# Kernel optimization log

Hardware: AMD Instinct MI355X
Metric: run time of the kernel (lower is better)

## Reference

```python
import jax, jax.numpy as jnp
import numpy as np

STATE_DIM = 512
N_AGENTS = 16
N_ACTIONS = 32
EMBED = 512          # mixing_embed_dim
Q_IN = STATE_DIM + N_AGENTS * N_ACTIONS  # 1024 (coma_critic arch)
ROWS = 32768         # bs * ts = 64 * 512


def _linear_params(key, d_in, d_out):
    kw, kb = jax.random.split(key)
    bound = 1.0 / np.sqrt(d_in)
    W = jax.random.uniform(kw, (d_in, d_out), minval=-bound, maxval=bound, dtype=jnp.float32)
    b = jax.random.uniform(kb, (d_out,), minval=-bound, maxval=bound, dtype=jnp.float32)
    return W, b


def setup_inputs() -> dict:
    key = jax.random.key(0)
    ks = jax.random.split(key, 8)
    states = jax.random.normal(ks[0], (ROWS, STATE_DIM), dtype=jnp.float32)
    actions = jax.random.uniform(ks[1], (ROWS, N_AGENTS * N_ACTIONS), dtype=jnp.float32)
    Qw1, Qb1 = _linear_params(ks[2], Q_IN, EMBED)
    Qw2, Qb2 = _linear_params(ks[3], EMBED, EMBED)
    Qw3, Qb3 = _linear_params(ks[4], EMBED, 1)
    Vw1, Vb1 = _linear_params(ks[5], STATE_DIM, EMBED)
    Vw2, Vb2 = _linear_params(ks[6], EMBED, EMBED)
    Vw3, Vb3 = _linear_params(ks[7], EMBED, 1)
    return {
        "states": states, "actions": actions,
        "Qw1": Qw1, "Qb1": Qb1, "Qw2": Qw2, "Qb2": Qb2, "Qw3": Qw3, "Qb3": Qb3,
        "Vw1": Vw1, "Vb1": Vb1, "Vw2": Vw2, "Vb2": Vb2, "Vw3": Vw3, "Vb3": Vb3,
    }


def _mlp3(x, W1, b1, W2, b2, W3, b3):
    h = jax.nn.relu(x @ W1 + b1)
    h = jax.nn.relu(h @ W2 + b2)
    return h @ W3 + b3


def reference(states, actions,
              Qw1, Qb1, Qw2, Qb2, Qw3, Qb3,
              Vw1, Vb1, Vw2, Vb2, Vw3, Vb3):
    # coma_critic arch: inputs = cat([states, joint-action one-hots], dim=1)
    inputs = jnp.concatenate([states, actions], axis=1)  # [bs*ts, Q_IN]
    q_outputs = _mlp3(inputs, Qw1, Qb1, Qw2, Qb2, Qw3, Qb3)  # [bs*ts, 1]
    v_outputs = _mlp3(states, Vw1, Vb1, Vw2, Vb2, Vw3, Vb3)  # [bs*ts, 1]
    return q_outputs, v_outputs
```

## Files before the change

kernel.cpp:

```cpp
#include <hip/hip_runtime.h>


#define ROWS 32768
#define EMBED 512

using frag_ab = __attribute__((ext_vector_type(8))) short;
using f32x4   = __attribute__((ext_vector_type(4))) float;

__device__ __forceinline__ unsigned short f2bf(float f) {
    unsigned int u = __builtin_bit_cast(unsigned int, f);
    return (unsigned short)((u + 0x7fffu + ((u >> 16) & 1u)) >> 16);
}

__device__ __forceinline__ unsigned pk2rne(float lo, float hi) {
    return (unsigned)f2bf(lo) | ((unsigned)f2bf(hi) << 16);
}

__device__ __forceinline__ void async_copy16(const void* g, void* l) {
    __builtin_amdgcn_global_load_lds(
        (const __attribute__((address_space(1))) unsigned int*)g,
        (__attribute__((address_space(3))) unsigned int*)l, 16, 0, 0);
}

__device__ __forceinline__ void decode_mn(int L, int& mi, int& nq) {
    nq = (L >> 3) & 3;
    mi = ((L >> 5) << 3) | (L & 7);
}

__global__ __launch_bounds__(256)
void prep(const float* __restrict__ states, const float* __restrict__ actions,
          const float* __restrict__ Qw1, const float* __restrict__ Qw2,
          const float* __restrict__ Vw1, const float* __restrict__ Vw2,
          const float* __restrict__ qb3, const float* __restrict__ vb3,
          unsigned short* __restrict__ X,
          unsigned short* __restrict__ Qw1t, unsigned short* __restrict__ Qw2t,
          unsigned short* __restrict__ Vw1t, unsigned short* __restrict__ Vw2t,
          float* __restrict__ out) {
    const int b = blockIdx.x, tid = threadIdx.x;
    if (b < 4096) {
        int c = b * 256 + tid;
        int m = c >> 5, col = (c & 31) * 32;
        const float* src = (col < 512) ? states + (size_t)m * 512 + col
                                       : actions + (size_t)m * 512 + (col - 512);
        float4 f[8];
#pragma unroll
        for (int i = 0; i < 8; i++) f[i] = ((const float4*)src)[i];
        uint4* dst = (uint4*)(X + (size_t)m * 1024 + col);
#pragma unroll
        for (int i = 0; i < 4; i++)
            dst[i] = make_uint4(pk2rne(f[2*i].x,   f[2*i].y),
                                pk2rne(f[2*i].z,   f[2*i].w),
                                pk2rne(f[2*i+1].x, f[2*i+1].y),
                                pk2rne(f[2*i+1].z, f[2*i+1].w));
    } else if (b < 4736) {
        int g = (b - 4096) * 256 + tid;
        const float* W; unsigned short* O; int n, k0, ldo;
        if (g < 65536) {
            int o = g * 8; n = o >> 10; k0 = o & 1023; W = Qw1; O = Qw1t; ldo = 1024;
        } else {
            g -= 65536;
            int seg = g >> 15, r = g & 32767, o = r * 8;
            n = o >> 9; k0 = o & 511; ldo = 512;
            W = (seg == 0) ? Qw2 : (seg == 1) ? Vw1 : Vw2;
            O = (seg == 0) ? Qw2t : (seg == 1) ? Vw1t : Vw2t;
        }
        float v[8];
#pragma unroll
        for (int j = 0; j < 8; j++) v[j] = W[(size_t)(k0 + j) * 512 + n];
        *(uint4*)(O + (size_t)n * ldo + k0) =
            make_uint4(pk2rne(v[0], v[1]), pk2rne(v[2], v[3]),
                       pk2rne(v[4], v[5]), pk2rne(v[6], v[7]));
    } else {
        int i = (b - 4736) * 256 + tid;
        out[i] = (i < ROWS) ? qb3[0] : vb3[0];
    }
}

__global__ __launch_bounds__(256, 2)
void layer1(const unsigned short* __restrict__ X,
            const unsigned short* __restrict__ Qw1t,
            const unsigned short* __restrict__ Vw1t,
            const float* __restrict__ Qb1, const float* __restrict__ Vb1,
            unsigned short* __restrict__ h1Q, unsigned short* __restrict__ h1V) {
    __shared__ __align__(16) unsigned short As[2 * 4096];
    __shared__ __align__(16) unsigned short Bs[2 * 8192];

    const int tid = threadIdx.x, wave = tid >> 6, lane = tid & 63;
    int mi, nq; decode_mn(blockIdx.x, mi, nq);
    const bool isV = nq >= 2;
    const int bn = (nq & 1) * 256;
    const int bm = mi * 128;
    const int K = isV ? 512 : 1024;
    const unsigned short* Wt = isV ? Vw1t : Qw1t;
    const float* bias = isV ? Vb1 : Qb1;
    unsigned short* H = isV ? h1V : h1Q;

    const int wm = (wave & 1) * 64, wn = (wave >> 1) * 128;
    const int lrow = lane & 15, quad = lane >> 4;
    f32x4 acc[4][8] = {};

    const int lin  = wave * 1024 + lane * 16;
    const int rowS = lin >> 6, colS = (lin & 63) >> 1;
    const unsigned short* gA0 = X + (size_t)(bm + rowS)      * 1024 + colS;
    const unsigned short* gA1 = X + (size_t)(bm + rowS + 64) * 1024 + colS;
    const unsigned short* gB0 = Wt + (size_t)(bn + rowS)       * K + colS;
    const unsigned short* gB1 = Wt + (size_t)(bn + rowS + 64)  * K + colS;
    const unsigned short* gB2 = Wt + (size_t)(bn + rowS + 128) * K + colS;
    const unsigned short* gB3 = Wt + (size_t)(bn + rowS + 192) * K + colS;
    unsigned short* ldsA0 = As + wave * 512;
    unsigned short* ldsA1 = As + 2048 + wave * 512;
    unsigned short* ldsB0 = Bs + wave * 512;
    unsigned short* ldsB1 = Bs + 2048 + wave * 512;
    unsigned short* ldsB2 = Bs + 4096 + wave * 512;
    unsigned short* ldsB3 = Bs + 6144 + wave * 512;

    for (int k0 = 0; k0 < K; k0 += 64) {
        async_copy16(gA0,      ldsA0);
        async_copy16(gA0 + 32, ldsA0 + 4096);
        async_copy16(gA1,      ldsA1);
        async_copy16(gA1 + 32, ldsA1 + 4096);
        async_copy16(gB0,      ldsB0);
        async_copy16(gB0 + 32, ldsB0 + 8192);
        async_copy16(gB1,      ldsB1);
        async_copy16(gB1 + 32, ldsB1 + 8192);
        async_copy16(gB2,      ldsB2);
        async_copy16(gB2 + 32, ldsB2 + 8192);
        async_copy16(gB3,      ldsB3);
        async_copy16(gB3 + 32, ldsB3 + 8192);
        gA0 += 64; gA1 += 64; gB0 += 64; gB1 += 64; gB2 += 64; gB3 += 64;
        __syncthreads();

#pragma unroll
        for (int s = 0; s < 2; s++) {
            frag_ab af[4], bfr[8];
#pragma unroll
            for (int i = 0; i < 4; i++)
                af[i] = *(const frag_ab*)&As[s * 4096 + (wm + i * 16 + lrow) * 32 + quad * 8];
#pragma unroll
            for (int j = 0; j < 8; j++)
                bfr[j] = *(const frag_ab*)&Bs[s * 8192 + (wn + j * 16 + lrow) * 32 + quad * 8];
#pragma unroll
            for (int i = 0; i < 4; i++)
#pragma unroll
                for (int j = 0; j < 8; j++)
                    acc[i][j] = __builtin_amdgcn_mfma_f32_16x16x32_bf16(
                        af[i], bfr[j], acc[i][j], 0, 0, 0);
        }
        __syncthreads();
    }

#pragma unroll
    for (int j = 0; j < 8; j++) {
        const int col = bn + wn + j * 16 + lrow;
        const float bc = bias[col];
#pragma unroll
        for (int i = 0; i < 4; i++) {
            const int row0 = bm + wm + i * 16 + quad * 4;
#pragma unroll
            for (int r = 0; r < 4; r++) {
                float v = acc[i][j][r] + bc;
                v = v > 0.0f ? v : 0.0f;
                H[(size_t)(row0 + r) * EMBED + col] = f2bf(v);
            }
        }
    }
}

__global__ __launch_bounds__(256, 2)
void layer2(const unsigned short* __restrict__ h1Q,
            const unsigned short* __restrict__ h1V,
            const unsigned short* __restrict__ Qw2t,
            const unsigned short* __restrict__ Vw2t,
            const float* __restrict__ Qb2, const float* __restrict__ Vb2,
            const float* __restrict__ Qw3, const float* __restrict__ Vw3,
            float* __restrict__ out) {
    __shared__ __align__(16) unsigned short As[2 * 4096];
    __shared__ __align__(16) unsigned short Bs[2 * 8192];

    const int tid = threadIdx.x, wave = tid >> 6, lane = tid & 63;
    int mi, nq; decode_mn(blockIdx.x, mi, nq);
    const bool isV = nq >= 2;
    const int bn = (nq & 1) * 256;
    const int bm = mi * 128;
    const unsigned short* A  = isV ? h1V : h1Q;
    const unsigned short* Wt = isV ? Vw2t : Qw2t;
    const float* bias = isV ? Vb2 : Qb2;
    const float* w3   = isV ? Vw3 : Qw3;
    float* op = out + (isV ? ROWS : 0);

    const int wm = (wave & 1) * 64, wn = (wave >> 1) * 128;
    const int lrow = lane & 15, quad = lane >> 4;
    f32x4 acc[4][8] = {};

    const int lin  = wave * 1024 + lane * 16;
    const int rowS = lin >> 6, colS = (lin & 63) >> 1;
    const unsigned short* gA0 = A + (size_t)(bm + rowS)      * 512 + colS;
    const unsigned short* gA1 = A + (size_t)(bm + rowS + 64) * 512 + colS;
    const unsigned short* gB0 = Wt + (size_t)(bn + rowS)       * 512 + colS;
    const unsigned short* gB1 = Wt + (size_t)(bn + rowS + 64)  * 512 + colS;
    const unsigned short* gB2 = Wt + (size_t)(bn + rowS + 128) * 512 + colS;
    const unsigned short* gB3 = Wt + (size_t)(bn + rowS + 192) * 512 + colS;
    unsigned short* ldsA0 = As + wave * 512;
    unsigned short* ldsA1 = As + 2048 + wave * 512;
    unsigned short* ldsB0 = Bs + wave * 512;
    unsigned short* ldsB1 = Bs + 2048 + wave * 512;
    unsigned short* ldsB2 = Bs + 4096 + wave * 512;
    unsigned short* ldsB3 = Bs + 6144 + wave * 512;

    for (int k0 = 0; k0 < 512; k0 += 64) {
        async_copy16(gA0,      ldsA0);
        async_copy16(gA0 + 32, ldsA0 + 4096);
        async_copy16(gA1,      ldsA1);
        async_copy16(gA1 + 32, ldsA1 + 4096);
        async_copy16(gB0,      ldsB0);
        async_copy16(gB0 + 32, ldsB0 + 8192);
        async_copy16(gB1,      ldsB1);
        async_copy16(gB1 + 32, ldsB1 + 8192);
        async_copy16(gB2,      ldsB2);
        async_copy16(gB2 + 32, ldsB2 + 8192);
        async_copy16(gB3,      ldsB3);
        async_copy16(gB3 + 32, ldsB3 + 8192);
        gA0 += 64; gA1 += 64; gB0 += 64; gB1 += 64; gB2 += 64; gB3 += 64;
        __syncthreads();

#pragma unroll
        for (int s = 0; s < 2; s++) {
            frag_ab af[4], bfr[8];
#pragma unroll
            for (int i = 0; i < 4; i++)
                af[i] = *(const frag_ab*)&As[s * 4096 + (wm + i * 16 + lrow) * 32 + quad * 8];
#pragma unroll
            for (int j = 0; j < 8; j++)
                bfr[j] = *(const frag_ab*)&Bs[s * 8192 + (wn + j * 16 + lrow) * 32 + quad * 8];
#pragma unroll
            for (int i = 0; i < 4; i++)
#pragma unroll
                for (int j = 0; j < 8; j++)
                    acc[i][j] = __builtin_amdgcn_mfma_f32_16x16x32_bf16(
                        af[i], bfr[j], acc[i][j], 0, 0, 0);
        }
        __syncthreads();
    }

    float bc[8], wc[8];
#pragma unroll
    for (int j = 0; j < 8; j++) {
        const int col = bn + wn + j * 16 + lrow;
        bc[j] = bias[col];
        wc[j] = w3[col];
    }
#pragma unroll
    for (int i = 0; i < 4; i++) {
#pragma unroll
        for (int r = 0; r < 4; r++) {
            float s = 0.0f;
#pragma unroll
            for (int j = 0; j < 8; j++) {
                float v = acc[i][j][r] + bc[j];
                v = v > 0.0f ? v : 0.0f;
                s += v * wc[j];
            }
#pragma unroll
            for (int m = 1; m < 16; m <<= 1) s += __shfl_xor(s, m, 64);
            if (lrow == 0)
                atomicAdd(&op[bm + wm + i * 16 + quad * 4 + r], s);
        }
    }
}

extern "C" void kernel_launch(void* const* d_in, const int* in_sizes, int n_in,
                              void* d_out, int out_size, void* d_ws, size_t ws_size,
                              hipStream_t stream) {
    const float* states  = (const float*)d_in[0];
    const float* actions = (const float*)d_in[1];
    const float* Qw1 = (const float*)d_in[2];
    const float* Qb1 = (const float*)d_in[3];
    const float* Qw2 = (const float*)d_in[4];
    const float* Qb2 = (const float*)d_in[5];
    const float* Qw3 = (const float*)d_in[6];
    const float* Qb3 = (const float*)d_in[7];
    const float* Vw1 = (const float*)d_in[8];
    const float* Vb1 = (const float*)d_in[9];
    const float* Vw2 = (const float*)d_in[10];
    const float* Vb2 = (const float*)d_in[11];
    const float* Vw3 = (const float*)d_in[12];
    const float* Vb3 = (const float*)d_in[13];
    float* out = (float*)d_out;

    char* ws = (char*)d_ws;
    unsigned short* X    = (unsigned short*)ws;
    unsigned short* h1Q  = (unsigned short*)(ws + 67108864);
    unsigned short* h1V  = (unsigned short*)(ws + 100663296);
    unsigned short* Qw1t = (unsigned short*)(ws + 134217728);
    unsigned short* Qw2t = Qw1t + 512 * 1024;
    unsigned short* Vw1t = Qw2t + 512 * 512;
    unsigned short* Vw2t = Vw1t + 512 * 512;

    prep<<<dim3(4992), dim3(256), 0, stream>>>(states, actions, Qw1, Qw2, Vw1, Vw2,
                                               Qb3, Vb3, X, Qw1t, Qw2t, Vw1t, Vw2t, out);

    layer1<<<dim3(1024), dim3(256), 0, stream>>>(X, Qw1t, Vw1t, Qb1, Vb1, h1Q, h1V);
    layer2<<<dim3(1024), dim3(256), 0, stream>>>(h1Q, h1V, Qw2t, Vw2t, Qb2, Vb2, Qw3, Vw3, out);
}
```

Measured before the change: 287.7 us.

## Rewrite GEMMs with 256x256 tiles, swizzled double-buffered LDS, and tiled weight transpose

The layer1 and layer2 GEMMs now use a shared 256x256-tile routine run by 512 threads. It double-buffers 128KB of LDS with XOR-swizzled rows to avoid bank conflicts, and interleaves the staging of the next tile with four quarter-MFMA phases that raise wave priority. Weight transposition in prep now goes through a 64x64 shared-memory tile, so global reads and writes are coalesced instead of strided. The block-to-work mapping also changes to group tiles. The risks are 128KB of LDS per block, which limits occupancy to one block per CU despite the launch bound, and heavy barrier use.

```diff
diff --git a/kernel.cpp b/kernel.cpp
--- a/kernel.cpp
+++ b/kernel.cpp
@@ -22,10 +22,10 @@
         (__attribute__((address_space(3))) unsigned int*)l, 16, 0, 0);
 }
 
-__device__ __forceinline__ void decode_mn(int L, int& mi, int& nq) {
-    nq = (L >> 3) & 3;
-    mi = ((L >> 5) << 3) | (L & 7);
-}
+#define VM0()   asm volatile("s_waitcnt vmcnt(0)" ::: "memory")
+#define LGKM0() asm volatile("s_waitcnt lgkmcnt(0)" ::: "memory")
+#define SBAR()  __builtin_amdgcn_s_barrier()
+#define SCHED0() __builtin_amdgcn_sched_barrier(0)
 
 __global__ __launch_bounds__(256)
 void prep(const float* __restrict__ states, const float* __restrict__ actions,
@@ -52,121 +52,189 @@
                                 pk2rne(f[2*i].z,   f[2*i].w),
                                 pk2rne(f[2*i+1].x, f[2*i+1].y),
                                 pk2rne(f[2*i+1].z, f[2*i+1].w));
-    } else if (b < 4736) {
-        int g = (b - 4096) * 256 + tid;
-        const float* W; unsigned short* O; int n, k0, ldo;
-        if (g < 65536) {
-            int o = g * 8; n = o >> 10; k0 = o & 1023; W = Qw1; O = Qw1t; ldo = 1024;
-        } else {
-            g -= 65536;
-            int seg = g >> 15, r = g & 32767, o = r * 8;
-            n = o >> 9; k0 = o & 511; ldo = 512;
+    } else if (b < 4416) {
+        __shared__ float T[64][65];
+        int tg = b - 4096;
+        const float* W; unsigned short* O; int Krows, kt, nt;
+        if (tg < 128) { W = Qw1; O = Qw1t; Krows = 1024; kt = tg >> 3; nt = tg & 7; }
+        else {
+            tg -= 128; int seg = tg >> 6, r = tg & 63;
+            kt = r >> 3; nt = r & 7; Krows = 512;
             W = (seg == 0) ? Qw2 : (seg == 1) ? Vw1 : Vw2;
             O = (seg == 0) ? Qw2t : (seg == 1) ? Vw1t : Vw2t;
         }
-        float v[8];
-#pragma unroll
-        for (int j = 0; j < 8; j++) v[j] = W[(size_t)(k0 + j) * 512 + n];
-        *(uint4*)(O + (size_t)n * ldo + k0) =
-            make_uint4(pk2rne(v[0], v[1]), pk2rne(v[2], v[3]),
-                       pk2rne(v[4], v[5]), pk2rne(v[6], v[7]));
+        const int k0 = kt * 64, n0 = nt * 64;
+        const int rr = tid >> 4, c4 = (tid & 15) * 4;
+#pragma unroll
+        for (int p = 0; p < 4; ++p) {
+            float4 v = *(const float4*)&W[(size_t)(k0 + p * 16 + rr) * 512 + n0 + c4];
+            T[p * 16 + rr][c4]     = v.x;
+            T[p * 16 + rr][c4 + 1] = v.y;
+            T[p * 16 + rr][c4 + 2] = v.z;
+            T[p * 16 + rr][c4 + 3] = v.w;
+        }
+        __syncthreads();
+        const int n = tid >> 2, kc = (tid & 3) * 16;
+        unsigned pk[8];
+#pragma unroll
+        for (int j = 0; j < 8; ++j)
+            pk[j] = pk2rne(T[kc + 2 * j][n], T[kc + 2 * j + 1][n]);
+        uint4* dst = (uint4*)(O + (size_t)(n0 + n) * Krows + k0 + kc);
+        dst[0] = make_uint4(pk[0], pk[1], pk[2], pk[3]);
+        dst[1] = make_uint4(pk[4], pk[5], pk[6], pk[7]);
     } else {
-        int i = (b - 4736) * 256 + tid;
+        int i = (b - 4416) * 256 + tid;
         out[i] = (i < ROWS) ? qb3[0] : vb3[0];
     }
 }
 
-__global__ __launch_bounds__(256, 2)
+__device__ __forceinline__ void gemm_256(
+    const unsigned short* __restrict__ A, int ldaE,
+    const unsigned short* __restrict__ Bt, int ldbE,
+    int K, int bm, int bn, char* smb, f32x4 acc[8][4])
+{
+    const int tid = threadIdx.x, wave = tid >> 6, lane = tid & 63;
+    const int im = wave >> 2, in = wave & 3;
+    const int lrow = lane & 15, quad = lane >> 4;
+    const int ldaB = ldaE * 2, ldbB = ldbE * 2;
+
+    const int srow = wave * 8 + (lane >> 3);
+    const int scol = (((lane & 7) ^ ((lane >> 3) & 7)) << 4);
+    const char* gA = (const char*)A + (size_t)(bm + srow) * ldaB + scol;
+    const char* gB = (const char*)Bt + (size_t)(bn + srow) * ldbB + scol;
+    char* ldsAw = smb + wave * 1024;
+    char* ldsBw = smb + 65536 + wave * 1024;
+
+    auto stageA = [&](int b, int h) {
+        const char* g = gA + (size_t)(h * 128) * ldaB;
+        char* l = ldsAw + b * 32768 + h * 16384;
+        async_copy16(g, l);
+        async_copy16(g + (size_t)64 * ldaB, l + 8192);
+    };
+    auto stageB = [&](int b, int h) {
+        const char* g = gB + (size_t)(h * 128) * ldbB;
+        char* l = ldsBw + b * 32768 + h * 16384;
+        async_copy16(g, l);
+        async_copy16(g + (size_t)64 * ldbB, l + 8192);
+    };
+
+    frag_ab a[4][2], b0[2][2], b1[2][2];
+
+    auto readA = [&](int b, int mh) {
+        const char* base = smb + b * 32768 + im * 16384;
+#pragma unroll
+        for (int i = 0; i < 4; ++i) {
+            const int r = mh * 64 + i * 16 + lrow;
+#pragma unroll
+            for (int s = 0; s < 2; ++s)
+                a[i][s] = *(const frag_ab*)(base + r * 128 +
+                              (((s * 4 + quad) ^ (r & 7)) << 4));
+        }
+    };
+    auto readB = [&](int b, int nh, frag_ab bb[2][2]) {
+#pragma unroll
+        for (int j = 0; j < 2; ++j) {
+            const int nr = in * 64 + nh * 32 + j * 16 + lrow;
+            const char* base = smb + 65536 + b * 32768 + (nr >> 7) * 16384;
+            const int r = nr & 127;
+#pragma unroll
+            for (int s = 0; s < 2; ++s)
+                bb[j][s] = *(const frag_ab*)(base + r * 128 +
+                               (((s * 4 + quad) ^ (r & 7)) << 4));
+        }
+    };
+    auto mma = [&](int mh, int nh, frag_ab bb[2][2]) {
+        __builtin_amdgcn_s_setprio(1);
+#pragma unroll
+        for (int s = 0; s < 2; ++s)
+#pragma unroll
+            for (int i = 0; i < 4; ++i)
+#pragma unroll
+                for (int j = 0; j < 2; ++j)
+                    acc[mh * 4 + i][nh * 2 + j] =
+                        __builtin_amdgcn_mfma_f32_16x16x32_bf16(
+                            a[i][s], bb[j][s], acc[mh * 4 + i][nh * 2 + j],
+                            0, 0, 0);
+        __builtin_amdgcn_s_setprio(0);
+    };
+
+    stageA(0, 0); stageB(0, 0); stageB(0, 1); stageA(0, 1);
+    gA += 128; gB += 128;
+    VM0();
+    SBAR();
+
+    const int NT = K >> 6;
+    int buf = 0;
+    for (int t = 0; t < NT; ++t) {
+        const bool more = (t + 1 < NT);
+        const int nb = buf ^ 1;
+        readA(buf, 0); readB(buf, 0, b0);
+        if (more) { stageA(nb, 0); stageB(nb, 0); }
+        SBAR(); LGKM0(); SCHED0();
+        mma(0, 0, b0);
+        SBAR();
+        readB(buf, 1, b1);
+        if (more) stageB(nb, 1);
+        SBAR(); LGKM0(); SCHED0();
+        mma(0, 1, b1);
+        SBAR();
+        readA(buf, 1);
+        if (more) { stageA(nb, 1); gA += 128; gB += 128; }
+        SBAR(); LGKM0(); SCHED0();
+        mma(1, 1, b1);
+        SBAR();
+        SBAR(); LGKM0(); SCHED0();
+        mma(1, 0, b0);
+        if (more) VM0();
+        SBAR();
+        buf ^= 1;
+    }
+}
+
+__device__ __forceinline__ void decode_work(int bid, int& mi, int& v) {
+    int work = ((bid & 7) << 6) | (bid >> 3);
+    mi = work >> 2; v = work & 3;
+}
+
+__global__ __launch_bounds__(512, 2)
 void layer1(const unsigned short* __restrict__ X,
             const unsigned short* __restrict__ Qw1t,
             const unsigned short* __restrict__ Vw1t,
             const float* __restrict__ Qb1, const float* __restrict__ Vb1,
             unsigned short* __restrict__ h1Q, unsigned short* __restrict__ h1V) {
-    __shared__ __align__(16) unsigned short As[2 * 4096];
-    __shared__ __align__(16) unsigned short Bs[2 * 8192];
-
-    const int tid = threadIdx.x, wave = tid >> 6, lane = tid & 63;
-    int mi, nq; decode_mn(blockIdx.x, mi, nq);
-    const bool isV = nq >= 2;
-    const int bn = (nq & 1) * 256;
-    const int bm = mi * 128;
+    __shared__ __align__(16) char smem[131072];
+    int mi, v; decode_work(blockIdx.x, mi, v);
+    const bool isV = v >= 2;
+    const int bm = mi * 256, bn = (v & 1) * 256;
     const int K = isV ? 512 : 1024;
     const unsigned short* Wt = isV ? Vw1t : Qw1t;
     const float* bias = isV ? Vb1 : Qb1;
     unsigned short* H = isV ? h1V : h1Q;
 
-    const int wm = (wave & 1) * 64, wn = (wave >> 1) * 128;
+    f32x4 acc[8][4] = {};
+    gemm_256(X, 1024, Wt, K, K, bm, bn, smem, acc);
+
+    const int tid = threadIdx.x, wave = tid >> 6, lane = tid & 63;
+    const int im = wave >> 2, in = wave & 3;
     const int lrow = lane & 15, quad = lane >> 4;
-    f32x4 acc[4][8] = {};
-
-    const int lin  = wave * 1024 + lane * 16;
-    const int rowS = lin >> 6, colS = (lin & 63) >> 1;
-    const unsigned short* gA0 = X + (size_t)(bm + rowS)      * 1024 + colS;
-    const unsigned short* gA1 = X + (size_t)(bm + rowS + 64) * 1024 + colS;
-    const unsigned short* gB0 = Wt + (size_t)(bn + rowS)       * K + colS;
-    const unsigned short* gB1 = Wt + (size_t)(bn + rowS + 64)  * K + colS;
-    const unsigned short* gB2 = Wt + (size_t)(bn + rowS + 128) * K + colS;
-    const unsigned short* gB3 = Wt + (size_t)(bn + rowS + 192) * K + colS;
-    unsigned short* ldsA0 = As + wave * 512;
-    unsigned short* ldsA1 = As + 2048 + wave * 512;
-    unsigned short* ldsB0 = Bs + wave * 512;
-    unsigned short* ldsB1 = Bs + 2048 + wave * 512;
-    unsigned short* ldsB2 = Bs + 4096 + wave * 512;
-    unsigned short* ldsB3 = Bs + 6144 + wave * 512;
-
-    for (int k0 = 0; k0 < K; k0 += 64) {
-        async_copy16(gA0,      ldsA0);
-        async_copy16(gA0 + 32, ldsA0 + 4096);
-        async_copy16(gA1,      ldsA1);
-        async_copy16(gA1 + 32, ldsA1 + 4096);
-        async_copy16(gB0,      ldsB0);
-        async_copy16(gB0 + 32, ldsB0 + 8192);
-        async_copy16(gB1,      ldsB1);
-        async_copy16(gB1 + 32, ldsB1 + 8192);
-        async_copy16(gB2,      ldsB2);
-        async_copy16(gB2 + 32, ldsB2 + 8192);
-        async_copy16(gB3,      ldsB3);
-        async_copy16(gB3 + 32, ldsB3 + 8192);
-        gA0 += 64; gA1 += 64; gB0 += 64; gB1 += 64; gB2 += 64; gB3 += 64;
-        __syncthreads();
-
-#pragma unroll
-        for (int s = 0; s < 2; s++) {
-            frag_ab af[4], bfr[8];
-#pragma unroll
-            for (int i = 0; i < 4; i++)
-                af[i] = *(const frag_ab*)&As[s * 4096 + (wm + i * 16 + lrow) * 32 + quad * 8];
-#pragma unroll
-            for (int j = 0; j < 8; j++)
-                bfr[j] = *(const frag_ab*)&Bs[s * 8192 + (wn + j * 16 + lrow) * 32 + quad * 8];
-#pragma unroll
-            for (int i = 0; i < 4; i++)
-#pragma unroll
-                for (int j = 0; j < 8; j++)
-                    acc[i][j] = __builtin_amdgcn_mfma_f32_16x16x32_bf16(
-                        af[i], bfr[j], acc[i][j], 0, 0, 0);
-        }
-        __syncthreads();
-    }
-
-#pragma unroll
-    for (int j = 0; j < 8; j++) {
-        const int col = bn + wn + j * 16 + lrow;
+#pragma unroll
+    for (int j = 0; j < 4; ++j) {
+        const int col = bn + in * 64 + j * 16 + lrow;
         const float bc = bias[col];
 #pragma unroll
-        for (int i = 0; i < 4; i++) {
-            const int row0 = bm + wm + i * 16 + quad * 4;
-#pragma unroll
-            for (int r = 0; r < 4; r++) {
-                float v = acc[i][j][r] + bc;
-                v = v > 0.0f ? v : 0.0f;
-                H[(size_t)(row0 + r) * EMBED + col] = f2bf(v);
+        for (int i = 0; i < 8; ++i) {
+            const int row0 = bm + im * 128 + i * 16 + quad * 4;
+#pragma unroll
+            for (int r = 0; r < 4; ++r) {
+                float val = acc[i][j][r] + bc;
+                val = val > 0.0f ? val : 0.0f;
+                H[(size_t)(row0 + r) * EMBED + col] = f2bf(val);
             }
         }
     }
 }
 
-__global__ __launch_bounds__(256, 2)
+__global__ __launch_bounds__(512, 2)
 void layer2(const unsigned short* __restrict__ h1Q,
             const unsigned short* __restrict__ h1V,
             const unsigned short* __restrict__ Qw2t,
@@ -174,96 +242,44 @@
             const float* __restrict__ Qb2, const float* __restrict__ Vb2,
             const float* __restrict__ Qw3, const float* __restrict__ Vw3,
             float* __restrict__ out) {
-    __shared__ __align__(16) unsigned short As[2 * 4096];
-    __shared__ __align__(16) unsigned short Bs[2 * 8192];
-
-    const int tid = threadIdx.x, wave = tid >> 6, lane = tid & 63;
-    int mi, nq; decode_mn(blockIdx.x, mi, nq);
-    const bool isV = nq >= 2;
-    const int bn = (nq & 1) * 256;
-    const int bm = mi * 128;
+    __shared__ __align__(16) char smem[131072];
+    int mi, v; decode_work(blockIdx.x, mi, v);
+    const bool isV = v >= 2;
+    const int bm = mi * 256, bn = (v & 1) * 256;
     const unsigned short* A  = isV ? h1V : h1Q;
     const unsigned short* Wt = isV ? Vw2t : Qw2t;
     const float* bias = isV ? Vb2 : Qb2;
     const float* w3   = isV ? Vw3 : Qw3;
     float* op = out + (isV ? ROWS : 0);
 
-    const int wm = (wave & 1) * 64, wn = (wave >> 1) * 128;
+    f32x4 acc[8][4] = {};
+    gemm_256(A, 512, Wt, 512, 512, bm, bn, smem, acc);
+
+    const int tid = threadIdx.x, wave = tid >> 6, lane = tid & 63;
+    const int im = wave >> 2, in = wave & 3;
     const int lrow = lane & 15, quad = lane >> 4;
-    f32x4 acc[4][8] = {};
-
-    const int lin  = wave * 1024 + lane * 16;
-    const int rowS = lin >> 6, colS = (lin & 63) >> 1;
-    const unsigned short* gA0 = A + (size_t)(bm + rowS)      * 512 + colS;
-    const unsigned short* gA1 = A + (size_t)(bm + rowS + 64) * 512 + colS;
-    const unsigned short* gB0 = Wt + (size_t)(bn + rowS)       * 512 + colS;
-    const unsigned short* gB1 = Wt + (size_t)(bn + rowS + 64)  * 512 + colS;
-    const unsigned short* gB2 = Wt + (size_t)(bn + rowS + 128) * 512 + colS;
-    const unsigned short* gB3 = Wt + (size_t)(bn + rowS + 192) * 512 + colS;
-    unsigned short* ldsA0 = As + wave * 512;
-    unsigned short* ldsA1 = As + 2048 + wave * 512;
-    unsigned short* ldsB0 = Bs + wave * 512;
-    unsigned short* ldsB1 = Bs + 2048 + wave * 512;
-    unsigned short* ldsB2 = Bs + 4096 + wave * 512;
-    unsigned short* ldsB3 = Bs + 6144 + wave * 512;
-
-    for (int k0 = 0; k0 < 512; k0 += 64) {
-        async_copy16(gA0,      ldsA0);
-        async_copy16(gA0 + 32, ldsA0 + 4096);
-        async_copy16(gA1,      ldsA1);
-        async_copy16(gA1 + 32, ldsA1 + 4096);
-        async_copy16(gB0,      ldsB0);
-        async_copy16(gB0 + 32, ldsB0 + 8192);
-        async_copy16(gB1,      ldsB1);
-        async_copy16(gB1 + 32, ldsB1 + 8192);
-        async_copy16(gB2,      ldsB2);
-        async_copy16(gB2 + 32, ldsB2 + 8192);
-        async_copy16(gB3,      ldsB3);
-        async_copy16(gB3 + 32, ldsB3 + 8192);
-        gA0 += 64; gA1 += 64; gB0 += 64; gB1 += 64; gB2 += 64; gB3 += 64;
-        __syncthreads();
-
-#pragma unroll
-        for (int s = 0; s < 2; s++) {
-            frag_ab af[4], bfr[8];
-#pragma unroll
-            for (int i = 0; i < 4; i++)
-                af[i] = *(const frag_ab*)&As[s * 4096 + (wm + i * 16 + lrow) * 32 + quad * 8];
-#pragma unroll
-            for (int j = 0; j < 8; j++)
-                bfr[j] = *(const frag_ab*)&Bs[s * 8192 + (wn + j * 16 + lrow) * 32 + quad * 8];
-#pragma unroll
-            for (int i = 0; i < 4; i++)
-#pragma unroll
-                for (int j = 0; j < 8; j++)
-                    acc[i][j] = __builtin_amdgcn_mfma_f32_16x16x32_bf16(
-                        af[i], bfr[j], acc[i][j], 0, 0, 0);
-        }
-        __syncthreads();
-    }
-
-    float bc[8], wc[8];
-#pragma unroll
-    for (int j = 0; j < 8; j++) {
-        const int col = bn + wn + j * 16 + lrow;
+    float bc[4], wc[4];
+#pragma unroll
+    for (int j = 0; j < 4; ++j) {
+        const int col = bn + in * 64 + j * 16 + lrow;
         bc[j] = bias[col];
         wc[j] = w3[col];
     }
 #pragma unroll
-    for (int i = 0; i < 4; i++) {
-#pragma unroll
-        for (int r = 0; r < 4; r++) {
+    for (int i = 0; i < 8; ++i) {
+#pragma unroll
+        for (int r = 0; r < 4; ++r) {
             float s = 0.0f;
 #pragma unroll
-            for (int j = 0; j < 8; j++) {
-                float v = acc[i][j][r] + bc[j];
-                v = v > 0.0f ? v : 0.0f;
-                s += v * wc[j];
+            for (int j = 0; j < 4; ++j) {
+                float val = acc[i][j][r] + bc[j];
+                val = val > 0.0f ? val : 0.0f;
+                s += val * wc[j];
             }
 #pragma unroll
             for (int m = 1; m < 16; m <<= 1) s += __shfl_xor(s, m, 64);
             if (lrow == 0)
-                atomicAdd(&op[bm + wm + i * 16 + quad * 4 + r], s);
+                atomicAdd(&op[bm + im * 128 + i * 16 + quad * 4 + r], s);
         }
     }
 }
@@ -296,9 +312,9 @@
     unsigned short* Vw1t = Qw2t + 512 * 512;
     unsigned short* Vw2t = Vw1t + 512 * 512;
 
-    prep<<<dim3(4992), dim3(256), 0, stream>>>(states, actions, Qw1, Qw2, Vw1, Vw2,
+    prep<<<dim3(4672), dim3(256), 0, stream>>>(states, actions, Qw1, Qw2, Vw1, Vw2,
                                                Qb3, Vb3, X, Qw1t, Qw2t, Vw1t, Vw2t, out);
 
-    layer1<<<dim3(1024), dim3(256), 0, stream>>>(X, Qw1t, Vw1t, Qb1, Vb1, h1Q, h1V);
-    layer2<<<dim3(1024), dim3(256), 0, stream>>>(h1Q, h1V, Qw2t, Vw2t, Qb2, Vb2, Qw3, Vw3, out);
-}
+    layer1<<<dim3(512), dim3(512), 0, stream>>>(X, Qw1t, Vw1t, Qb1, Vb1, h1Q, h1V);
+    layer2<<<dim3(512), dim3(512), 0, stream>>>(h1Q, h1V, Qw2t, Vw2t, Qb2, Vb2, Qw3, Vw3, out);
+}
```

Measured after the change: 289.6 us. About the same (+0.7%).
